# Kernel tuning notes

Measured on AMD Instinct MI355X. Metric: run time of the kernel, lower is better.

## Reference

```python
import jax, jax.numpy as jnp
import numpy as np

N_NODES = 50000


def gcn_conv(x, edge_index, W, b, n_nodes):
    """GCNConv: out = D^-1/2 (A + I) D^-1/2 (x W) + b (symmetric norm, self-loops)."""
    src, dst = edge_index[0], edge_index[1]
    loop = jnp.arange(n_nodes, dtype=src.dtype)
    src = jnp.concatenate([src, loop])  # [E + N]
    dst = jnp.concatenate([dst, loop])
    deg = jax.ops.segment_sum(jnp.ones_like(dst, dtype=x.dtype), dst,
                              num_segments=n_nodes)
    dinv = jnp.where(deg > 0, jax.lax.rsqrt(deg), 0.0)
    norm = dinv[src] * dinv[dst]  # [E + N]
    h = x @ W  # [N, out_dim]
    msg = h[src] * norm[:, None]  # gather + scale, [E + N, out_dim]
    out = jax.ops.segment_sum(msg, dst, num_segments=n_nodes)  # scatter-add
    return out + b


def batch_norm(x, gamma, beta, eps=1e-5):
    mean = jnp.mean(x, axis=0)
    var = jnp.var(x, axis=0)
    return (x - mean) * jax.lax.rsqrt(var + eps) * gamma + beta


def setup_inputs() -> dict:
    key = jax.random.key(0)
    ks = jax.random.split(key, 6)
    in_c, hid, lat = 64, 128, 64
    x = jax.random.normal(ks[0], (N_NODES, in_c), dtype=jnp.float32)
    edge_index = jax.random.randint(ks[1], (2, 1600000), 0, N_NODES, dtype=jnp.int64)
    W1 = jax.random.normal(ks[2], (in_c, hid), dtype=jnp.float32) * (1.0 / np.sqrt(in_c))
    b1 = jnp.zeros((hid,), dtype=jnp.float32)
    gamma = jnp.ones((hid,), dtype=jnp.float32)
    beta = jnp.zeros((hid,), dtype=jnp.float32)
    W2 = jax.random.normal(ks[3], (hid, lat), dtype=jnp.float32) * (1.0 / np.sqrt(hid))
    b2 = jnp.zeros((lat,), dtype=jnp.float32)
    return {"x": x, "edge_index": edge_index, "W1": W1, "b1": b1,
            "gamma": gamma, "beta": beta, "W2": W2, "b2": b2}


def reference(x, edge_index, W1, b1, gamma, beta, W2, b2):
    h = gcn_conv(x, edge_index, W1, b1, N_NODES)
    h = batch_norm(h, gamma, beta)
    h = jax.nn.relu(h)
    # dropout omitted (deterministic reference; identity in expectation-free eval)
    return gcn_conv(h, edge_index, W2, b2, N_NODES)
```

## Files before the change

### kernel.cpp

```cpp
#include <hip/hip_runtime.h>

#define N_NODES 50000
#define C1 64
#define C2 128
#define C3 64
#define NBUCK ((N_NODES + 63) / 64)
#define BCAP 8192
#define STILE 4096

__device__ __forceinline__ float bf2f(unsigned short u) {
    union { unsigned int i; float f; } v; v.i = ((unsigned int)u) << 16; return v.f;
}
__device__ __forceinline__ unsigned short f2bf(float f) {
    union { float f; unsigned int i; } v; v.f = f;
    return (unsigned short)((v.i + 0x7FFFu + ((v.i >> 16) & 1u)) >> 16);
}
__device__ __forceinline__ float hi2f(unsigned int p) {
    union { unsigned int i; float f; } v; v.i = p & 0xFFFF0000u; return v.f;
}

__global__ void k_zero_cast(const float* __restrict__ x, unsigned short* __restrict__ xh,
                            int* __restrict__ bcount, float* __restrict__ stats) {
    int i = blockIdx.x * blockDim.x + threadIdx.x;
    if (i < NBUCK) bcount[i] = 0;
    if (i < 512) stats[i] = 0.0f;
    if (i < N_NODES * C1 / 4) {
        float4 v = ((const float4*)x)[i];
        ushort4 o;
        o.x = f2bf(v.x); o.y = f2bf(v.y); o.z = f2bf(v.z); o.w = f2bf(v.w);
        ((ushort4*)xh)[i] = o;
    }
}

__global__ __launch_bounds__(256) void k_hist(const int* __restrict__ dst, int E,
                                              int* __restrict__ bcount) {
    __shared__ int lh[NBUCK];
    int tid = threadIdx.x;
    for (int i = tid; i < NBUCK; i += 256) lh[i] = 0;
    __syncthreads();
    int stride = gridDim.x * blockDim.x;
    for (int e = blockIdx.x * blockDim.x + tid; e < E; e += stride)
        atomicAdd(&lh[dst[e] >> 6], 1);
    __syncthreads();
    for (int i = tid; i < NBUCK; i += 256)
        if (lh[i]) atomicAdd(&bcount[i], lh[i]);
}

__global__ __launch_bounds__(1024) void k_scanb(const int* __restrict__ bcount,
                                                int* __restrict__ bstart,
                                                int* __restrict__ bcursor) {
    __shared__ int sums[1024];
    int t = threadIdx.x;
    int v = (t < NBUCK) ? bcount[t] : 0;
    sums[t] = v;
    __syncthreads();
    for (int off = 1; off < 1024; off <<= 1) {
        int u = (t >= off) ? sums[t - off] : 0;
        __syncthreads();
        sums[t] += u;
        __syncthreads();
    }
    if (t < NBUCK) {
        int ex = sums[t] - v;
        bstart[t] = ex;
        bcursor[t * 16] = ex;
    }
}

__global__ __launch_bounds__(256) void k_scatterc(const int* __restrict__ src,
                                                  const int* __restrict__ dst, int E,
                                                  int* __restrict__ bcursor,
                                                  int* __restrict__ pairs) {
    __shared__ int lh[NBUCK];
    __shared__ int gbase[NBUCK];
    int tid = threadIdx.x;
    int base = blockIdx.x * STILE;
    for (int i = tid; i < NBUCK; i += 256) lh[i] = 0;
    __syncthreads();
    int sv[16], dv[16], rk[16];
#pragma unroll
    for (int k = 0; k < 16; ++k) {
        int e = base + k * 256 + tid;
        sv[k] = -1;
        if (e < E) {
            sv[k] = src[e];
            dv[k] = dst[e];
            rk[k] = atomicAdd(&lh[dv[k] >> 6], 1);
        }
    }
    __syncthreads();
    for (int i = tid; i < NBUCK; i += 256) {
        int c = lh[i];
        gbase[i] = c ? atomicAdd(&bcursor[i * 16], c) : 0;
    }
    __syncthreads();
#pragma unroll
    for (int k = 0; k < 16; ++k) {
        if (sv[k] >= 0) {
            int b = dv[k] >> 6;
            pairs[gbase[b] + rk[k]] = (sv[k] << 6) | (dv[k] & 63);
        }
    }
}

__global__ __launch_bounds__(256) void k_refine(const int* __restrict__ bstart,
                                                const int* __restrict__ bcount,
                                                int* __restrict__ rowstart,
                                                float* __restrict__ dinv,
                                                int* __restrict__ pairs) {
    __shared__ int stage[BCAP];
    __shared__ int lcnt[64];
    __shared__ int lcur[64];
    int b = blockIdx.x;
    int tid = threadIdx.x;
    int e0 = bstart[b], n = bcount[b];
    if (tid < 64) lcnt[tid] = 0;
    __syncthreads();
    for (int j = tid; j < n; j += 256) {
        int pk = pairs[e0 + j];
        stage[j] = pk;
        atomicAdd(&lcnt[pk & 63], 1);
    }
    __syncthreads();
    if (tid < 64) {
        int dg = lcnt[tid];
        int pfx = dg;
#pragma unroll
        for (int off = 1; off < 64; off <<= 1) {
            int v = __shfl_up(pfx, off);
            if (tid >= off) pfx += v;
        }
        int st = e0 + (pfx - dg);
        int nd = b * 64 + tid;
        rowstart[nd] = st;
        dinv[nd] = rsqrtf(1.0f + (float)dg);
        lcur[tid] = st;
    }
    __syncthreads();
    for (int j = tid; j < n; j += 256) {
        int pk = stage[j];
        int pos = atomicAdd(&lcur[pk & 63], 1);
        pairs[pos] = pk >> 6;
    }
}

__global__ void k_pack(const int* __restrict__ csr, const float* __restrict__ dinv,
                       unsigned int* __restrict__ wsrc, int E) {
    int j = blockIdx.x * blockDim.x + threadIdx.x;
    if (j < E) {
        int s = csr[j];
        wsrc[j] = ((unsigned int)f2bf(dinv[s]) << 16) | (unsigned int)s;
    }
}

__global__ __launch_bounds__(256) void k_pullx(const int* __restrict__ rowstart,
                                               const unsigned int* __restrict__ wsrc,
                                               const float* __restrict__ x,
                                               const unsigned short* __restrict__ xh,
                                               const float* __restrict__ dinv,
                                               float* __restrict__ aggx) {
    int node = blockIdx.x * 4 + (threadIdx.x >> 6);
    if (node >= N_NODES) return;
    int lane = threadIdx.x & 63;
    int start = rowstart[node], end = rowstart[node + 1];
    float dd = dinv[node];
    float a0 = 0.0f, a1 = 0.0f, a2 = 0.0f, a3 = 0.0f;
    int j = start;
    for (; j + 3 < end; j += 4) {
        unsigned int p0 = wsrc[j],     p1 = wsrc[j + 1];
        unsigned int p2 = wsrc[j + 2], p3 = wsrc[j + 3];
        float v0 = bf2f(xh[(p0 & 0xFFFFu) * C1 + lane]);
        float v1 = bf2f(xh[(p1 & 0xFFFFu) * C1 + lane]);
        float v2 = bf2f(xh[(p2 & 0xFFFFu) * C1 + lane]);
        float v3 = bf2f(xh[(p3 & 0xFFFFu) * C1 + lane]);
        a0 = fmaf(v0, hi2f(p0), a0); a1 = fmaf(v1, hi2f(p1), a1);
        a2 = fmaf(v2, hi2f(p2), a2); a3 = fmaf(v3, hi2f(p3), a3);
    }
    for (; j < end; ++j) {
        unsigned int p = wsrc[j];
        a0 = fmaf(bf2f(xh[(p & 0xFFFFu) * C1 + lane]), hi2f(p), a0);
    }
    float eacc = (a0 + a1) + (a2 + a3);
    aggx[node * C1 + lane] = fmaf(x[node * C1 + lane], dd * dd, dd * eacc);
}

__global__ __launch_bounds__(256) void k_gemm1b(const float* __restrict__ aggx,
                                                const float* __restrict__ W1,
                                                const float* __restrict__ b1,
                                                float* __restrict__ agg1) {
    __shared__ float Ws[C1 * C2];
    __shared__ float Xs[32 * C1];
    int tid = threadIdx.x;
    int r0 = blockIdx.x * 32;
    for (int i = tid; i < C1 * C2; i += 256) Ws[i] = W1[i];
    for (int i = tid; i < 32 * C1; i += 256) {
        int row = r0 + (i >> 6);
        Xs[i] = (row < N_NODES) ? aggx[row * C1 + (i & 63)] : 0.0f;
    }
    __syncthreads();
    int c = tid & 127;
    int rg = tid >> 7;
    float bv = b1[c];
    float acc[16];
#pragma unroll
    for (int r = 0; r < 16; ++r) acc[r] = 0.0f;
    for (int k = 0; k < C1; ++k) {
        float w = Ws[k * C2 + c];
#pragma unroll
        for (int r = 0; r < 16; ++r)
            acc[r] = fmaf(Xs[(rg * 16 + r) * C1 + k], w, acc[r]);
    }
#pragma unroll
    for (int r = 0; r < 16; ++r) {
        int row = r0 + rg * 16 + r;
        if (row < N_NODES) agg1[row * C2 + c] = acc[r] + bv;
    }
}

__global__ __launch_bounds__(256) void k_stats(const float* __restrict__ agg1,
                                               float* __restrict__ stats) {
    __shared__ float ls[256], lq[256];
    int tid = threadIdx.x;
    int c = tid & 127, half = tid >> 7;
    float s = 0.0f, q = 0.0f;
    for (int row = blockIdx.x * 2 + half; row < N_NODES; row += gridDim.x * 2) {
        float v = agg1[row * C2 + c];
        s += v; q += v * v;
    }
    ls[tid] = s; lq[tid] = q;
    __syncthreads();
    if (tid < 128) {
        s = ls[tid] + ls[tid + 128];
        q = lq[tid] + lq[tid + 128];
        unsafeAtomicAdd(&stats[c], s);
        unsafeAtomicAdd(&stats[128 + c], q);
    }
}

__global__ void k_bnparam(const float* __restrict__ gamma, const float* __restrict__ beta,
                          float* __restrict__ stats) {
    int c = threadIdx.x;
    if (c < 128) {
        const float invN = 1.0f / (float)N_NODES;
        float mean = stats[c] * invN;
        float var = stats[128 + c] * invN - mean * mean;
        float sc = gamma[c] * rsqrtf(var + 1e-5f);
        stats[256 + c] = sc;
        stats[384 + c] = beta[c] - mean * sc;
    }
}

__global__ __launch_bounds__(256) void k_gemm2(const float* __restrict__ agg1,
                                               const float* __restrict__ W2,
                                               const float* __restrict__ stats,
                                               unsigned short* __restrict__ h2h) {
    __shared__ float Ws[C2 * C3];
    __shared__ float As[32 * C2];
    int tid = threadIdx.x;
    int r0 = blockIdx.x * 32;
    for (int i = tid; i < C2 * C3; i += 256) Ws[i] = W2[i];
    for (int i = tid; i < 32 * C2; i += 256) {
        int row = r0 + (i >> 7);
        int cc = i & 127;
        float v = 0.0f;
        if (row < N_NODES)
            v = fmaxf(fmaf(agg1[row * C2 + cc], stats[256 + cc], stats[384 + cc]), 0.0f);
        As[i] = v;
    }
    __syncthreads();
    int c = tid & 63;
    int rg = tid >> 6;
    float acc[8];
#pragma unroll
    for (int r = 0; r < 8; ++r) acc[r] = 0.0f;
    for (int k = 0; k < C2; ++k) {
        float w = Ws[k * C3 + c];
#pragma unroll
        for (int r = 0; r < 8; ++r)
            acc[r] = fmaf(As[(rg * 8 + r) * C2 + k], w, acc[r]);
    }
#pragma unroll
    for (int r = 0; r < 8; ++r) {
        int row = r0 + rg * 8 + r;
        if (row < N_NODES) h2h[row * C3 + c] = f2bf(acc[r]);
    }
}

__global__ __launch_bounds__(256) void k_pull2(const int* __restrict__ rowstart,
                                               const unsigned int* __restrict__ wsrc,
                                               const unsigned short* __restrict__ h2h,
                                               const float* __restrict__ dinv,
                                               const float* __restrict__ b2,
                                               float* __restrict__ out) {
    int node = blockIdx.x * 4 + (threadIdx.x >> 6);
    if (node >= N_NODES) return;
    int lane = threadIdx.x & 63;
    int start = rowstart[node], end = rowstart[node + 1];
    float dd = dinv[node];
    float a0 = 0.0f, a1 = 0.0f, a2 = 0.0f, a3 = 0.0f;
    int j = start;
    for (; j + 3 < end; j += 4) {
        unsigned int p0 = wsrc[j],     p1 = wsrc[j + 1];
        unsigned int p2 = wsrc[j + 2], p3 = wsrc[j + 3];
        float v0 = bf2f(h2h[(p0 & 0xFFFFu) * C3 + lane]);
        float v1 = bf2f(h2h[(p1 & 0xFFFFu) * C3 + lane]);
        float v2 = bf2f(h2h[(p2 & 0xFFFFu) * C3 + lane]);
        float v3 = bf2f(h2h[(p3 & 0xFFFFu) * C3 + lane]);
        a0 = fmaf(v0, hi2f(p0), a0); a1 = fmaf(v1, hi2f(p1), a1);
        a2 = fmaf(v2, hi2f(p2), a2); a3 = fmaf(v3, hi2f(p3), a3);
    }
    for (; j < end; ++j) {
        unsigned int p = wsrc[j];
        a0 = fmaf(bf2f(h2h[(p & 0xFFFFu) * C3 + lane]), hi2f(p), a0);
    }
    float eacc = (a0 + a1) + (a2 + a3);
    float self = bf2f(h2h[node * C3 + lane]);
    out[node * C3 + lane] = b2[lane] + fmaf(self, dd * dd, dd * eacc);
}

extern "C" void kernel_launch(void* const* d_in, const int* in_sizes, int n_in,
                              void* d_out, int out_size, void* d_ws, size_t ws_size,
                              hipStream_t stream) {
    const float* x     = (const float*)d_in[0];
    const int*   ei    = (const int*)d_in[1];
    const float* W1    = (const float*)d_in[2];
    const float* b1    = (const float*)d_in[3];
    const float* gamma = (const float*)d_in[4];
    const float* beta  = (const float*)d_in[5];
    const float* W2    = (const float*)d_in[6];
    const float* b2    = (const float*)d_in[7];
    float* out = (float*)d_out;

    int E = in_sizes[1] / 2;
    const int* src = ei;
    const int* dst = ei + E;

    char* ws = (char*)d_ws;
    float*          dinv     = (float*)ws;
    float*          stats    = (float*)(ws + 200704);
    int*            bcount   = (int*)(ws + 202752);
    int*            bstart   = (int*)(ws + 206848);
    int*            bcursor  = (int*)(ws + 210944);
    int*            rowstart = (int*)(ws + 261120);
    int*            pairs    = (int*)(ws + 461824);
    unsigned int*   wsrc     = (unsigned int*)(ws + 6861824);
    unsigned short* xh       = (unsigned short*)(ws + 13261824);
    float*          aggx     = (float*)(ws + 19661824);
    float*          agg1     = (float*)(ws + 32461824);
    unsigned short* h2h      = (unsigned short*)(ws + 58061824);

    const int nblk_cast  = (N_NODES * C1 / 4 + 255) / 256;
    const int nblk_rows  = (N_NODES + 31) / 32;
    const int nblk_scat  = (E + STILE - 1) / STILE;
    const int nblk_edge  = (E + 255) / 256;
    const int nblk_pull  = (N_NODES + 3) / 4;

    k_zero_cast<<<nblk_cast, 256, 0, stream>>>(x, xh, bcount, stats);
    k_hist<<<256, 256, 0, stream>>>(dst, E, bcount);
    k_scanb<<<1, 1024, 0, stream>>>(bcount, bstart, bcursor);
    k_scatterc<<<nblk_scat, 256, 0, stream>>>(src, dst, E, bcursor, pairs);
    k_refine<<<NBUCK, 256, 0, stream>>>(bstart, bcount, rowstart, dinv, pairs);
    k_pack<<<nblk_edge, 256, 0, stream>>>(pairs, dinv, wsrc, E);

    k_pullx<<<nblk_pull, 256, 0, stream>>>(rowstart, wsrc, x, xh, dinv, aggx);
    k_gemm1b<<<nblk_rows, 256, 0, stream>>>(aggx, W1, b1, agg1);

    k_stats<<<256, 256, 0, stream>>>(agg1, stats);
    k_bnparam<<<1, 128, 0, stream>>>(gamma, beta, stats);

    k_gemm2<<<nblk_rows, 256, 0, stream>>>(agg1, W2, stats, h2h);
    k_pull2<<<nblk_pull, 256, 0, stream>>>(rowstart, wsrc, h2h, dinv, b2, out);
}
```

Baseline: 349.3 us.

## Drop the dst histogram pass with fixed-capacity buckets, and stage edge words in LDS

The separate histogram and pre-scan over dst are removed. Edges are now scattered straight into fixed-capacity per-bucket regions (BCAP slots each), using the bucket cursors as counters, and the scan over the final counts runs after the scatter to give compacted CSR offsets. This saves one full read of dst and a kernel launch, but it assumes no bucket of 64 destination nodes gets more than BCAP edges. The two pull kernels now load up to 64 packed edge words per wave with one coalesced load into LDS, instead of per-edge uniform loads. Workspace buffers are re-aliased so the CSR and bucket arrays share space with later activation buffers.

Measured after the change: 314.5 us. 10.0% less time.

```diff
diff --git a/kernel.cpp b/kernel.cpp
--- a/kernel.cpp
+++ b/kernel.cpp
@@ -4,8 +4,8 @@
 #define C1 64
 #define C2 128
 #define C3 64
-#define NBUCK ((N_NODES + 63) / 64)
-#define BCAP 8192
+#define NBUCK 782
+#define BCAP 8160
 #define STILE 4096
 
 __device__ __forceinline__ float bf2f(unsigned short u) {
@@ -20,50 +20,15 @@
 }
 
 __global__ void k_zero_cast(const float* __restrict__ x, unsigned short* __restrict__ xh,
-                            int* __restrict__ bcount, float* __restrict__ stats) {
+                            int* __restrict__ bcursor, float* __restrict__ stats) {
     int i = blockIdx.x * blockDim.x + threadIdx.x;
-    if (i < NBUCK) bcount[i] = 0;
+    if (i < NBUCK * 16) bcursor[i] = 0;
     if (i < 512) stats[i] = 0.0f;
     if (i < N_NODES * C1 / 4) {
         float4 v = ((const float4*)x)[i];
         ushort4 o;
         o.x = f2bf(v.x); o.y = f2bf(v.y); o.z = f2bf(v.z); o.w = f2bf(v.w);
         ((ushort4*)xh)[i] = o;
-    }
-}
-
-__global__ __launch_bounds__(256) void k_hist(const int* __restrict__ dst, int E,
-                                              int* __restrict__ bcount) {
-    __shared__ int lh[NBUCK];
-    int tid = threadIdx.x;
-    for (int i = tid; i < NBUCK; i += 256) lh[i] = 0;
-    __syncthreads();
-    int stride = gridDim.x * blockDim.x;
-    for (int e = blockIdx.x * blockDim.x + tid; e < E; e += stride)
-        atomicAdd(&lh[dst[e] >> 6], 1);
-    __syncthreads();
-    for (int i = tid; i < NBUCK; i += 256)
-        if (lh[i]) atomicAdd(&bcount[i], lh[i]);
-}
-
-__global__ __launch_bounds__(1024) void k_scanb(const int* __restrict__ bcount,
-                                                int* __restrict__ bstart,
-                                                int* __restrict__ bcursor) {
-    __shared__ int sums[1024];
-    int t = threadIdx.x;
-    int v = (t < NBUCK) ? bcount[t] : 0;
-    sums[t] = v;
-    __syncthreads();
-    for (int off = 1; off < 1024; off <<= 1) {
-        int u = (t >= off) ? sums[t - off] : 0;
-        __syncthreads();
-        sums[t] += u;
-        __syncthreads();
-    }
-    if (t < NBUCK) {
-        int ex = sums[t] - v;
-        bstart[t] = ex;
-        bcursor[t * 16] = ex;
     }
 }
 
@@ -98,26 +63,45 @@
     for (int k = 0; k < 16; ++k) {
         if (sv[k] >= 0) {
             int b = dv[k] >> 6;
-            pairs[gbase[b] + rk[k]] = (sv[k] << 6) | (dv[k] & 63);
-        }
-    }
-}
-
-__global__ __launch_bounds__(256) void k_refine(const int* __restrict__ bstart,
-                                                const int* __restrict__ bcount,
+            pairs[b * BCAP + gbase[b] + rk[k]] = (sv[k] << 6) | (dv[k] & 63);
+        }
+    }
+}
+
+__global__ __launch_bounds__(1024) void k_scanb(const int* __restrict__ bcursor,
+                                                int* __restrict__ cbase) {
+    __shared__ int sums[1024];
+    int t = threadIdx.x;
+    int v = (t < NBUCK) ? bcursor[t * 16] : 0;
+    sums[t] = v;
+    __syncthreads();
+    for (int off = 1; off < 1024; off <<= 1) {
+        int u = (t >= off) ? sums[t - off] : 0;
+        __syncthreads();
+        sums[t] += u;
+        __syncthreads();
+    }
+    if (t < NBUCK) cbase[t] = sums[t] - v;
+}
+
+__global__ __launch_bounds__(256) void k_refine(const int* __restrict__ bcursor,
+                                                const int* __restrict__ cbase,
                                                 int* __restrict__ rowstart,
                                                 float* __restrict__ dinv,
-                                                int* __restrict__ pairs) {
+                                                const int* __restrict__ pairs,
+                                                int* __restrict__ csr) {
     __shared__ int stage[BCAP];
     __shared__ int lcnt[64];
     __shared__ int lcur[64];
     int b = blockIdx.x;
     int tid = threadIdx.x;
-    int e0 = bstart[b], n = bcount[b];
+    int n = bcursor[b * 16];
+    int e0s = b * BCAP;
+    int c0 = cbase[b];
     if (tid < 64) lcnt[tid] = 0;
     __syncthreads();
     for (int j = tid; j < n; j += 256) {
-        int pk = pairs[e0 + j];
+        int pk = pairs[e0s + j];
         stage[j] = pk;
         atomicAdd(&lcnt[pk & 63], 1);
     }
@@ -130,7 +114,7 @@
             int v = __shfl_up(pfx, off);
             if (tid >= off) pfx += v;
         }
-        int st = e0 + (pfx - dg);
+        int st = c0 + (pfx - dg);
         int nd = b * 64 + tid;
         rowstart[nd] = st;
         dinv[nd] = rsqrtf(1.0f + (float)dg);
@@ -140,7 +124,7 @@
     for (int j = tid; j < n; j += 256) {
         int pk = stage[j];
         int pos = atomicAdd(&lcur[pk & 63], 1);
-        pairs[pos] = pk >> 6;
+        csr[pos] = pk >> 6;
     }
 }
 
@@ -159,26 +143,31 @@
                                                const unsigned short* __restrict__ xh,
                                                const float* __restrict__ dinv,
                                                float* __restrict__ aggx) {
-    int node = blockIdx.x * 4 + (threadIdx.x >> 6);
+    __shared__ unsigned int sp[4][64];
+    int wid = threadIdx.x >> 6, lane = threadIdx.x & 63;
+    int node = blockIdx.x * 4 + wid;
     if (node >= N_NODES) return;
-    int lane = threadIdx.x & 63;
     int start = rowstart[node], end = rowstart[node + 1];
     float dd = dinv[node];
     float a0 = 0.0f, a1 = 0.0f, a2 = 0.0f, a3 = 0.0f;
-    int j = start;
-    for (; j + 3 < end; j += 4) {
-        unsigned int p0 = wsrc[j],     p1 = wsrc[j + 1];
-        unsigned int p2 = wsrc[j + 2], p3 = wsrc[j + 3];
-        float v0 = bf2f(xh[(p0 & 0xFFFFu) * C1 + lane]);
-        float v1 = bf2f(xh[(p1 & 0xFFFFu) * C1 + lane]);
-        float v2 = bf2f(xh[(p2 & 0xFFFFu) * C1 + lane]);
-        float v3 = bf2f(xh[(p3 & 0xFFFFu) * C1 + lane]);
-        a0 = fmaf(v0, hi2f(p0), a0); a1 = fmaf(v1, hi2f(p1), a1);
-        a2 = fmaf(v2, hi2f(p2), a2); a3 = fmaf(v3, hi2f(p3), a3);
-    }
-    for (; j < end; ++j) {
-        unsigned int p = wsrc[j];
-        a0 = fmaf(bf2f(xh[(p & 0xFFFFu) * C1 + lane]), hi2f(p), a0);
+    for (int j0 = start; j0 < end; j0 += 64) {
+        int n = end - j0; if (n > 64) n = 64;
+        if (lane < n) sp[wid][lane] = wsrc[j0 + lane];
+        int k = 0;
+        for (; k + 3 < n; k += 4) {
+            unsigned int p0 = sp[wid][k],     p1 = sp[wid][k + 1];
+            unsigned int p2 = sp[wid][k + 2], p3 = sp[wid][k + 3];
+            float v0 = bf2f(xh[(p0 & 0xFFFFu) * C1 + lane]);
+            float v1 = bf2f(xh[(p1 & 0xFFFFu) * C1 + lane]);
+            float v2 = bf2f(xh[(p2 & 0xFFFFu) * C1 + lane]);
+            float v3 = bf2f(xh[(p3 & 0xFFFFu) * C1 + lane]);
+            a0 = fmaf(v0, hi2f(p0), a0); a1 = fmaf(v1, hi2f(p1), a1);
+            a2 = fmaf(v2, hi2f(p2), a2); a3 = fmaf(v3, hi2f(p3), a3);
+        }
+        for (; k < n; ++k) {
+            unsigned int p = sp[wid][k];
+            a0 = fmaf(bf2f(xh[(p & 0xFFFFu) * C1 + lane]), hi2f(p), a0);
+        }
     }
     float eacc = (a0 + a1) + (a2 + a3);
     aggx[node * C1 + lane] = fmaf(x[node * C1 + lane], dd * dd, dd * eacc);
@@ -292,26 +281,31 @@
                                                const float* __restrict__ dinv,
                                                const float* __restrict__ b2,
                                                float* __restrict__ out) {
-    int node = blockIdx.x * 4 + (threadIdx.x >> 6);
+    __shared__ unsigned int sp[4][64];
+    int wid = threadIdx.x >> 6, lane = threadIdx.x & 63;
+    int node = blockIdx.x * 4 + wid;
     if (node >= N_NODES) return;
-    int lane = threadIdx.x & 63;
     int start = rowstart[node], end = rowstart[node + 1];
     float dd = dinv[node];
     float a0 = 0.0f, a1 = 0.0f, a2 = 0.0f, a3 = 0.0f;
-    int j = start;
-    for (; j + 3 < end; j += 4) {
-        unsigned int p0 = wsrc[j],     p1 = wsrc[j + 1];
-        unsigned int p2 = wsrc[j + 2], p3 = wsrc[j + 3];
-        float v0 = bf2f(h2h[(p0 & 0xFFFFu) * C3 + lane]);
-        float v1 = bf2f(h2h[(p1 & 0xFFFFu) * C3 + lane]);
-        float v2 = bf2f(h2h[(p2 & 0xFFFFu) * C3 + lane]);
-        float v3 = bf2f(h2h[(p3 & 0xFFFFu) * C3 + lane]);
-        a0 = fmaf(v0, hi2f(p0), a0); a1 = fmaf(v1, hi2f(p1), a1);
-        a2 = fmaf(v2, hi2f(p2), a2); a3 = fmaf(v3, hi2f(p3), a3);
-    }
-    for (; j < end; ++j) {
-        unsigned int p = wsrc[j];
-        a0 = fmaf(bf2f(h2h[(p & 0xFFFFu) * C3 + lane]), hi2f(p), a0);
+    for (int j0 = start; j0 < end; j0 += 64) {
+        int n = end - j0; if (n > 64) n = 64;
+        if (lane < n) sp[wid][lane] = wsrc[j0 + lane];
+        int k = 0;
+        for (; k + 3 < n; k += 4) {
+            unsigned int p0 = sp[wid][k],     p1 = sp[wid][k + 1];
+            unsigned int p2 = sp[wid][k + 2], p3 = sp[wid][k + 3];
+            float v0 = bf2f(h2h[(p0 & 0xFFFFu) * C3 + lane]);
+            float v1 = bf2f(h2h[(p1 & 0xFFFFu) * C3 + lane]);
+            float v2 = bf2f(h2h[(p2 & 0xFFFFu) * C3 + lane]);
+            float v3 = bf2f(h2h[(p3 & 0xFFFFu) * C3 + lane]);
+            a0 = fmaf(v0, hi2f(p0), a0); a1 = fmaf(v1, hi2f(p1), a1);
+            a2 = fmaf(v2, hi2f(p2), a2); a3 = fmaf(v3, hi2f(p3), a3);
+        }
+        for (; k < n; ++k) {
+            unsigned int p = sp[wid][k];
+            a0 = fmaf(bf2f(h2h[(p & 0xFFFFu) * C3 + lane]), hi2f(p), a0);
+        }
     }
     float eacc = (a0 + a1) + (a2 + a3);
     float self = bf2f(h2h[node * C3 + lane]);
@@ -338,16 +332,16 @@
     char* ws = (char*)d_ws;
     float*          dinv     = (float*)ws;
     float*          stats    = (float*)(ws + 200704);
-    int*            bcount   = (int*)(ws + 202752);
-    int*            bstart   = (int*)(ws + 206848);
-    int*            bcursor  = (int*)(ws + 210944);
-    int*            rowstart = (int*)(ws + 261120);
-    int*            pairs    = (int*)(ws + 461824);
-    unsigned int*   wsrc     = (unsigned int*)(ws + 6861824);
-    unsigned short* xh       = (unsigned short*)(ws + 13261824);
-    float*          aggx     = (float*)(ws + 19661824);
-    float*          agg1     = (float*)(ws + 32461824);
-    unsigned short* h2h      = (unsigned short*)(ws + 58061824);
+    int*            bcursor  = (int*)(ws + 202752);
+    int*            cbase    = (int*)(ws + 252928);
+    int*            rowstart = (int*)(ws + 257024);
+    unsigned int*   wsrc     = (unsigned int*)(ws + 457728);
+    unsigned short* xh       = (unsigned short*)(ws + 6857728);
+    float*          aggx     = (float*)(ws + 13257728);
+    int*            csr      = (int*)(ws + 13257728);
+    float*          agg1     = (float*)(ws + 26057728);
+    int*            pairs    = (int*)(ws + 26057728);
+    unsigned short* h2h      = (unsigned short*)(ws + 51657728);
 
     const int nblk_cast  = (N_NODES * C1 / 4 + 255) / 256;
     const int nblk_rows  = (N_NODES + 31) / 32;
@@ -355,12 +349,11 @@
     const int nblk_edge  = (E + 255) / 256;
     const int nblk_pull  = (N_NODES + 3) / 4;
 
-    k_zero_cast<<<nblk_cast, 256, 0, stream>>>(x, xh, bcount, stats);
-    k_hist<<<256, 256, 0, stream>>>(dst, E, bcount);
-    k_scanb<<<1, 1024, 0, stream>>>(bcount, bstart, bcursor);
+    k_zero_cast<<<nblk_cast, 256, 0, stream>>>(x, xh, bcursor, stats);
     k_scatterc<<<nblk_scat, 256, 0, stream>>>(src, dst, E, bcursor, pairs);
-    k_refine<<<NBUCK, 256, 0, stream>>>(bstart, bcount, rowstart, dinv, pairs);
-    k_pack<<<nblk_edge, 256, 0, stream>>>(pairs, dinv, wsrc, E);
+    k_scanb<<<1, 1024, 0, stream>>>(bcursor, cbase);
+    k_refine<<<NBUCK, 256, 0, stream>>>(bcursor, cbase, rowstart, dinv, pairs, csr);
+    k_pack<<<nblk_edge, 256, 0, stream>>>(csr, dinv, wsrc, E);
 
     k_pullx<<<nblk_pull, 256, 0, stream>>>(rowstart, wsrc, x, xh, dinv, aggx);
     k_gemm1b<<<nblk_rows, 256, 0, stream>>>(aggx, W1, b1, agg1);
```
